# Kernel optimization log

Hardware: AMD Instinct MI355X
Metric: run time of the kernel (lower is better)

## Reference

```python
import jax, jax.numpy as jnp
import numpy as np

B, T, D_IN, H, C = 1024, 85, 20, 1024, 27
OBJ = T * 36  # flattened (T, 12, 3) object stream


def _mlp(h, W1, b1, W2, b2):
    # BaseEncoderDecoderLayout stand-in: Dense(H, relu) -> Dense(out)
    return jnp.maximum(h @ W1 + b1, 0.0) @ W2 + b2


def setup_inputs() -> dict:
    key = jax.random.key(0)
    ks = jax.random.split(key, 8)
    s = lambda k, shape: jax.random.normal(k, shape, jnp.float32) * 0.02
    return {
        "o": jax.random.normal(ks[0], (B, OBJ), jnp.float32),
        "x": jax.random.normal(ks[1], (B, T, D_IN), jnp.float32),
        # objProcess = BaseEncoderDecoderLayout(num_hid, dim_output=num_hid)
        "oW1": s(ks[2], (OBJ, H)), "ob1": jnp.zeros((H,), jnp.float32),
        "oW2": s(ks[3], (H, H)), "ob2": jnp.zeros((H,), jnp.float32),
        # expertWeightNet = BaseEncoderDecoderLayout(num_hid, dim_output=num_classes)
        "eW1": s(ks[4], (D_IN + H, H)), "eb1": jnp.zeros((H,), jnp.float32),
        "eW2": s(ks[5], (H, C)), "eb2": jnp.zeros((C,), jnp.float32),
    }


def reference(o, x, oW1, ob1, oW2, ob2, eW1, eb1, eW2, eb2):
    objInfo = _mlp(o, oW1, ob1, oW2, ob2)  # [B, H]

    def expert(cur):  # cur: [B, D_IN]
        return _mlp(jnp.concatenate([cur, objInfo], axis=-1), eW1, eb1, eW2, eb2)

    # step 0 uses raw x[:, 0, :]
    ew0 = expert(x[:, 0, :])  # [B, C]

    # steps 1..T-2: first feature of currentInput is replaced by previous
    # result's channel-0, i.e. result[:, -1, 0] -> sequential recurrence
    def step(prev, xt):  # prev: [B], xt: [B, D_IN]
        cur = jnp.concatenate([prev[:, None], xt[:, 1:]], axis=-1)
        ew = expert(cur)
        return ew[:, 0], ew

    xs = jnp.swapaxes(x[:, 1:T - 1, :], 0, 1)  # [T-2, B, D_IN]
    _, rest = jax.lax.scan(step, ew0[:, 0], xs)  # rest: [T-2, B, C]

    result = jnp.concatenate([ew0[None], rest], axis=0)  # [T-1, B, C]
    return jnp.swapaxes(result, 0, 1)  # [B, T-1, C]
```

## Files before the change

kernel.cpp:

```cpp
#include <hip/hip_runtime.h>
#include <hip/hip_bf16.h>

#define B_   1024
#define T_   85
#define DIN  20
#define H_   1024
#define C_   27
#define OBJ_ (T_ * 36)
#define TOUT (T_ - 1)

typedef unsigned short u16;
typedef __attribute__((ext_vector_type(8))) short bf16x8;
typedef __attribute__((ext_vector_type(4))) float f32x4;

__device__ __forceinline__ u16 f2bf(float f) {
    __hip_bfloat16 h = __float2bfloat16(f);
    return *reinterpret_cast<u16*>(&h);
}
__device__ __forceinline__ float bf2f(u16 u) {
    __hip_bfloat16 h;
    *reinterpret_cast<u16*>(&h) = u;
    return __bfloat162float(h);
}
__device__ __forceinline__ int f_as_i(float f) {
    union { float f; int i; } u; u.f = f; return u.i;
}
__device__ __forceinline__ float i_as_f(int i) {
    union { float f; int i; } u; u.i = i; return u.f;
}

__device__ __forceinline__ float wave64_sum_bcast(float p) {
    p += i_as_f(__builtin_amdgcn_update_dpp(0, f_as_i(p), 0x111, 0xf, 0xf, true));
    p += i_as_f(__builtin_amdgcn_update_dpp(0, f_as_i(p), 0x112, 0xf, 0xf, true));
    p += i_as_f(__builtin_amdgcn_update_dpp(0, f_as_i(p), 0x114, 0xf, 0xf, true));
    p += i_as_f(__builtin_amdgcn_update_dpp(0, f_as_i(p), 0x118, 0xf, 0xf, true));
    p += i_as_f(__builtin_amdgcn_update_dpp(0, f_as_i(p), 0x142, 0xa, 0xf, true));
    p += i_as_f(__builtin_amdgcn_update_dpp(0, f_as_i(p), 0x143, 0xc, 0xf, true));
    return i_as_f(__builtin_amdgcn_readlane(f_as_i(p), 63));
}

__global__ __launch_bounds__(256) void convertK2(
    const float* __restrict__ o, const float* __restrict__ oW1,
    const float* __restrict__ eW1, const float* __restrict__ oW2,
    const float* __restrict__ eW2, const float* __restrict__ ob2,
    u16* __restrict__ o_bf, u16* __restrict__ bW1t, u16* __restrict__ bE1t,
    u16* __restrict__ o2bf, u16* __restrict__ w2th,
    u16* __restrict__ e1t20, float* __restrict__ biasp)
{
    __shared__ float tl[64][65];
    const int bid = blockIdx.x, t = threadIdx.x;

    if (bid < 512) {
        for (int it = 0; it < 6; ++it) {
            const int idx = (bid * 256 + t) + it * 131072;
            const int row = idx / 768, g = idx - row * 768;
            float4 v = make_float4(0.f, 0.f, 0.f, 0.f);
            if (g < 765) v = *(const float4*)(o + (size_t)row * 3060 + g * 4);
            const float* vp = (const float*)&v;
            ushort4 uh;
            uh.x = f2bf(vp[0]); uh.y = f2bf(vp[1]);
            uh.z = f2bf(vp[2]); uh.w = f2bf(vp[3]);
            *(ushort4*)(o_bf + (size_t)row * 3072 + g * 4) = uh;
        }
    } else if (bid < 1536) {
        const bool isW1 = (bid < 1280);
        const int idx = isW1 ? (bid - 512) : (bid - 1280);
        const int k0 = (idx >> 4) * 64, n0 = (idx & 15) * 64;
        const float* src = isW1 ? oW1 : (eW1 + (size_t)DIN * H_);
        const int Ksrc = isW1 ? 3060 : 1024;
        u16* dst = isW1 ? bW1t : bE1t;
        const int ldk = isW1 ? 3072 : 1024;
#pragma unroll
        for (int r = 0; r < 4; ++r) {
            const int k = k0 + r * 16 + (t >> 4);
            float4 v = make_float4(0.f, 0.f, 0.f, 0.f);
            if (k < Ksrc)
                v = *(const float4*)(src + (size_t)k * 1024 + n0 + (t & 15) * 4);
            const float* vp = (const float*)&v;
#pragma unroll
            for (int j = 0; j < 4; ++j)
                tl[r * 16 + (t >> 4)][(t & 15) * 4 + j] = vp[j];
        }
        __syncthreads();
#pragma unroll
        for (int r = 0; r < 4; ++r) {
            const int n = r * 16 + (t >> 4);
            ushort4 u;
            u.x = f2bf(tl[(t & 15) * 4 + 0][n]);
            u.y = f2bf(tl[(t & 15) * 4 + 1][n]);
            u.z = f2bf(tl[(t & 15) * 4 + 2][n]);
            u.w = f2bf(tl[(t & 15) * 4 + 3][n]);
            *(ushort4*)(dst + (size_t)(n0 + n) * ldk + k0 + (t & 15) * 4) = u;
        }
    } else if (bid < 1664) {
        const int base = (bid - 1536) * 256 + t;
#pragma unroll
        for (int it = 0; it < 8; ++it) {
            const int g = base + it * 32768;
            float4 v = *(const float4*)(oW2 + (size_t)g * 4);
            const float* vp = (const float*)&v;
            ushort4 uh;
            uh.x = f2bf(vp[0]); uh.y = f2bf(vp[1]);
            uh.z = f2bf(vp[2]); uh.w = f2bf(vp[3]);
            *(ushort4*)(o2bf + (size_t)g * 4) = uh;
        }
    } else if (bid < 1696) {
        const int c = bid - 1664;
#pragma unroll
        for (int kk = 0; kk < 4; ++kk) {
            const int k = kk * 256 + t;
            const float v = (c < C_) ? eW2[(size_t)k * C_ + c] : 0.f;
            w2th[(size_t)c * 1024 + k] = f2bf(v);
        }
    } else if (bid < 1700) {
        const int n = (bid - 1696) * 256 + t;
        u16 buf[32];
#pragma unroll
        for (int k = 0; k < 32; ++k)
            buf[k] = (k < DIN) ? f2bf(eW1[(size_t)k * H_ + n]) : (u16)0;
#pragma unroll
        for (int q = 0; q < 4; ++q)
            *(uint4*)(e1t20 + (size_t)n * 32 + q * 8) = *(uint4*)&buf[q * 8];
    } else {
        const int r = bid - 1700, kc = r >> 2, nb = r & 3;
        const int n = nb * 256 + t;
        const int k0 = kc * 128;
        float acc = 0.f;
#pragma unroll 8
        for (int k = 0; k < 128; ++k)
            acc = fmaf(ob2[k0 + k], eW1[(size_t)(DIN + k0 + k) * H_ + n], acc);
        biasp[kc * H_ + n] = acc;
    }
}

template <int BN>
__device__ __forceinline__ void gemm_mfma_tile(
    const u16* __restrict__ A0, const u16* __restrict__ Bt,
    float* __restrict__ C, const float* __restrict__ bias,
    int ldK, int nk1, int gm0, int gn0, char* lds)
{
    constexpr int FN    = BN / 32;
    constexpr int WNw   = BN / 2;
    constexpr int BR    = BN / 64;
    constexpr int BUFSZ = 8192 + BN * 64;

    const int tid  = threadIdx.x;
    const int wave = tid >> 6, l = tid & 63, ml = l & 15, koct = l >> 4;
    const int wm = wave >> 1, wn = wave & 1;
    const int swz = koct ^ ((ml >> 1) & 3);
    const int a_ro = (wm * 64 + ml) * 64 + swz * 16;
    const int b_ro = (wn * WNw + ml) * 64 + swz * 16;

    const int sm = tid >> 2, sq = tid & 3;
    int wAo[2], wBo[BR];
    size_t gAo[2], gBo[BR];
#pragma unroll
    for (int q = 0; q < 2; ++q) {
        const int m = q * 64 + sm;
        wAo[q] = m * 64 + ((sq ^ ((m >> 1) & 3)) * 16);
        gAo[q] = (size_t)(gm0 + m) * ldK * 2 + sq * 16;
    }
#pragma unroll
    for (int q = 0; q < BR; ++q) {
        const int n = q * 64 + sm;
        wBo[q] = n * 64 + ((sq ^ ((n >> 1) & 3)) * 16);
        gBo[q] = (size_t)(gn0 + n) * ldK * 2 + sq * 16;
    }

    f32x4 acc[4][FN];
    const f32x4 zz = {0.f, 0.f, 0.f, 0.f};
#pragma unroll
    for (int i = 0; i < 4; ++i)
#pragma unroll
        for (int j = 0; j < FN; ++j) acc[i][j] = zz;

    const char* A0c = (const char*)A0;
    const char* Btc = (const char*)Bt;

    uint4 st[2 + BR];
    auto stage = [&](int kt) {
        const size_t koff = (size_t)kt * 64;
        st[0] = *(const uint4*)(A0c + gAo[0] + koff);
        st[1] = *(const uint4*)(A0c + gAo[1] + koff);
#pragma unroll
        for (int q = 0; q < BR; ++q)
            st[2 + q] = *(const uint4*)(Btc + gBo[q] + koff);
    };
    auto dswrite = [&](int buf) {
        char* d = lds + buf * BUFSZ;
        *(uint4*)(d + wAo[0]) = st[0];
        *(uint4*)(d + wAo[1]) = st[1];
#pragma unroll
        for (int q = 0; q < BR; ++q)
            *(uint4*)(d + 8192 + wBo[q]) = st[2 + q];
    };
    auto compute = [&](int buf) {
        const char* As = lds + buf * BUFSZ;
        const char* Bs = As + 8192;
        bf16x8 af[4], bfv[FN];
#pragma unroll
        for (int fm = 0; fm < 4; ++fm)
            af[fm] = *(const bf16x8*)(As + a_ro + fm * 1024);
#pragma unroll
        for (int fn = 0; fn < FN; ++fn)
            bfv[fn] = *(const bf16x8*)(Bs + b_ro + fn * 1024);
#pragma unroll
        for (int fm = 0; fm < 4; ++fm)
#pragma unroll
            for (int fn = 0; fn < FN; ++fn)
                acc[fm][fn] = __builtin_amdgcn_mfma_f32_16x16x32_bf16(
                    af[fm], bfv[fn], acc[fm][fn], 0, 0, 0);
    };

    stage(0); dswrite(0); __syncthreads();
    for (int kt = 0; kt < nk1; ++kt) {
        if (kt + 1 < nk1) stage(kt + 1);
        compute(kt & 1);
        if (kt + 1 < nk1) dswrite((kt + 1) & 1);
        __syncthreads();
    }

    float br[FN];
#pragma unroll
    for (int fn = 0; fn < FN; ++fn)
        br[fn] = bias ? bias[gn0 + wn * WNw + fn * 16 + ml] : 0.f;
#pragma unroll
    for (int fm = 0; fm < 4; ++fm) {
        const int rowb = gm0 + wm * 64 + fm * 16 + koct * 4;
#pragma unroll
        for (int fn = 0; fn < FN; ++fn) {
            const int col = gn0 + wn * WNw + fn * 16 + ml;
#pragma unroll
            for (int r = 0; r < 4; ++r)
                C[(size_t)(rowb + r) * 1024 + col] = acc[fm][fn][r] + br[fn];
        }
    }
}

__global__ __launch_bounds__(256) void kernelA2(
    const u16* __restrict__ o_bf, const u16* __restrict__ bW1t,
    const u16* __restrict__ o2bf, const u16* __restrict__ bE1t,
    float* __restrict__ p_h1, float* __restrict__ p_wc)
{
    __shared__ alignas(16) char lds[2 * 12288];
    const int bid = blockIdx.x;
    if (bid < 384) {
        const int c = bid >> 7, tl = bid & 127;
        gemm_mfma_tile<64>(o_bf + c * 1024, bW1t + c * 1024,
                           p_h1 + (size_t)c * 1048576, nullptr, 3072, 32,
                           (tl >> 4) * 128, (tl & 15) * 64, lds);
    } else {
        const int tl = bid - 384;
        gemm_mfma_tile<64>(o2bf, bE1t, p_wc, nullptr, 1024, 32,
                           (tl >> 4) * 128, (tl & 15) * 64, lds);
    }
}

__global__ __launch_bounds__(256) void epilogue2(
    const float* __restrict__ p_h1, const float* __restrict__ p_wc,
    const float* __restrict__ ob1, const float* __restrict__ eb1,
    const float* __restrict__ biasp,
    u16* __restrict__ h1bf, u16* __restrict__ Wct, float* __restrict__ biasWc)
{
    __shared__ float tl[64][65];
    const int bid = blockIdx.x, t = threadIdx.x;
    if (bid < 256) {
#pragma unroll
        for (int it = 0; it < 4; ++it) {
            const int g = bid * 1024 + it * 256 + t;
            const size_t e = (size_t)g * 4;
            float4 a = *(const float4*)(p_h1 + e);
            float4 b = *(const float4*)(p_h1 + 1048576 + e);
            float4 c = *(const float4*)(p_h1 + 2097152 + e);
            float4 s = *(const float4*)(ob1 + (e & 1023));
            const float *ap = (const float*)&a, *bp = (const float*)&b,
                        *cp = (const float*)&c, *sp = (const float*)&s;
            ushort4 uh;
            u16* up = (u16*)&uh;
#pragma unroll
            for (int j = 0; j < 4; ++j)
                up[j] = f2bf(fmaxf(ap[j] + bp[j] + cp[j] + sp[j], 0.f));
            *(ushort4*)(h1bf + e) = uh;
        }
    } else if (bid < 512) {
        const int idx = bid - 256;
        const int k0 = (idx >> 4) * 64, n0 = (idx & 15) * 64;
#pragma unroll
        for (int r = 0; r < 4; ++r) {
            const int k = k0 + r * 16 + (t >> 4);
            float4 v = *(const float4*)(p_wc + (size_t)k * 1024 + n0 + (t & 15) * 4);
            const float* vp = (const float*)&v;
#pragma unroll
            for (int j = 0; j < 4; ++j)
                tl[r * 16 + (t >> 4)][(t & 15) * 4 + j] = vp[j];
        }
        __syncthreads();
#pragma unroll
        for (int r = 0; r < 4; ++r) {
            const int n = r * 16 + (t >> 4);
            ushort4 u;
            u.x = f2bf(tl[(t & 15) * 4 + 0][n]);
            u.y = f2bf(tl[(t & 15) * 4 + 1][n]);
            u.z = f2bf(tl[(t & 15) * 4 + 2][n]);
            u.w = f2bf(tl[(t & 15) * 4 + 3][n]);
            *(ushort4*)(Wct + (size_t)(n0 + n) * 1024 + k0 + (t & 15) * 4) = u;
        }
    } else {
        const int j0 = t * 4;
        float4 s = *(const float4*)(eb1 + j0);
        float* sp = (float*)&s;
#pragma unroll
        for (int kc = 0; kc < 8; ++kc) {
            float4 p = *(const float4*)(biasp + kc * H_ + j0);
            const float* pp = (const float*)&p;
#pragma unroll
            for (int i = 0; i < 4; ++i) sp[i] += pp[i];
        }
        *(float4*)(biasWc + j0) = s;
    }
}

__global__ __launch_bounds__(256) void kernelB2(
    const u16* __restrict__ h1bf, const u16* __restrict__ Wct,
    const float* __restrict__ biasWc,
    float* __restrict__ base0, float* __restrict__ base1)
{
    __shared__ alignas(16) char lds[2 * 12288];
    const int bid = blockIdx.x;
    const int p = bid >> 7, tl = bid & 127;
    gemm_mfma_tile<64>(h1bf + p * 512, Wct + p * 512,
                       p ? base1 : base0, p ? biasWc : nullptr,
                       1024, 16, (tl >> 4) * 128, (tl & 15) * 64, lds);
}

#define CPH 8
#define CNPH 11

__global__ __launch_bounds__(256, 3) void chain_seq5(
    const float* __restrict__ x, const u16* __restrict__ e1t20,
    const float* __restrict__ eW1, const float* __restrict__ eW2,
    const float* __restrict__ eb2,
    const float* __restrict__ base0, const float* __restrict__ base1,
    float* __restrict__ cur0_buf)
{
    __shared__ u16   A_bf[2][CPH * 1032];
    __shared__ float base_s[1024];

    const int b = blockIdx.x, tid = threadIdx.x;
    const int w = tid >> 6, l = tid & 63;
    const int ml = l & 15, koct = l >> 4;

    {
        const int j = tid * 4;
        float4 b0v = *(const float4*)&base0[(size_t)b * H_ + j];
        float4 b1v = *(const float4*)&base1[(size_t)b * H_ + j];
        float4 s;
        s.x = b0v.x + b1v.x; s.y = b0v.y + b1v.y;
        s.z = b0v.z + b1v.z; s.w = b0v.w + b1v.w;
        *(float4*)&base_s[j] = s;
    }
    __syncthreads();

    const f32x4 zz = {0.f, 0.f, 0.f, 0.f};

    auto produce = [&](int ph) {
        const int t0 = ph * CPH;
        u16 hw[8];
        const int tg = t0 + ml;
        const bool rowok = (ml < CPH) && (tg < T_);
#pragma unroll
        for (int e = 0; e < 8; ++e) {
            const int k = koct * 8 + e;
            float vx = 0.f;
            if (rowok && k >= 1 && k < DIN)
                vx = x[(size_t)b * (T_ * DIN) + tg * DIN + k];
            hw[e] = f2bf(vx);
        }
        bf16x8 af;
        {
            uint4 pk;
            pk.x = hw[0] | ((unsigned)hw[1] << 16);
            pk.y = hw[2] | ((unsigned)hw[3] << 16);
            pk.z = hw[4] | ((unsigned)hw[5] << 16);
            pk.w = hw[6] | ((unsigned)hw[7] << 16);
            af = *(bf16x8*)&pk;
        }
        const int beg = (w == 1) ? 0 : (w == 2) ? 22 : 43;
        const int end = (w == 1) ? 22 : (w == 2) ? 43 : 64;
        u16* dst = A_bf[ph & 1];
#pragma unroll 2
        for (int jt = beg; jt < end; ++jt) {
            const bf16x8 bf = *(const bf16x8*)
                &e1t20[(size_t)(jt * 16 + ml) * 32 + koct * 8];
            f32x4 c = __builtin_amdgcn_mfma_f32_16x16x32_bf16(af, bf, zz, 0, 0, 0);
            if (koct < 2) {
                const int jcol = jt * 16 + ml;
                const float bj = base_s[jcol];
#pragma unroll
                for (int r = 0; r < 4; ++r)
                    dst[(koct * 4 + r) * 1032 + jcol] = f2bf(c[r] + bj);
            }
        }
    };

    float u[16], v[16];
    float prev = 0.f, cur0_init = 0.f;
    if (w) {
        produce(0);
    } else {
#pragma unroll
        for (int i = 0; i < 16; ++i) {
            const int j = i * 64 + l;
            u[i] = eW1[j];
            v[i] = eW2[(size_t)j * C_];
        }
        cur0_init = x[(size_t)b * (T_ * DIN)];
    }
    __syncthreads();

    const float eb20 = eb2[0];
    float* cb = cur0_buf + (size_t)b * TOUT;

#pragma unroll 1
    for (int ph = 0; ph < CNPH; ++ph) {
        if (w) {
            if (ph + 1 < CNPH) produce(ph + 1);
        } else {
            const int t0 = ph * CPH;
            const int rem = 83 - t0;
            const int nst = (rem < CPH) ? rem : CPH;
            const u16* Abuf = A_bf[ph & 1];

            float a_cur[16];
#pragma unroll
            for (int i = 0; i < 16; ++i)
                a_cur[i] = bf2f(Abuf[i * 64 + l]);

            for (int sl = 0; sl < nst; ++sl) {
                const int t = t0 + sl;
                const int sln = (sl + 1 < nst) ? sl + 1 : sl;
                float a_nxt[16];
#pragma unroll
                for (int i = 0; i < 16; ++i)
                    a_nxt[i] = bf2f(Abuf[sln * 1032 + i * 64 + l]);

                const float cur0 = (t == 0) ? cur0_init : prev;
                if (l == 0) cb[t] = cur0;

                float p0 = 0.f, p1 = 0.f, p2 = 0.f, p3 = 0.f;
#pragma unroll
                for (int i = 0; i < 16; i += 4) {
                    p0 = fmaf(fmaxf(fmaf(cur0, u[i + 0], a_cur[i + 0]), 0.f), v[i + 0], p0);
                    p1 = fmaf(fmaxf(fmaf(cur0, u[i + 1], a_cur[i + 1]), 0.f), v[i + 1], p1);
                    p2 = fmaf(fmaxf(fmaf(cur0, u[i + 2], a_cur[i + 2]), 0.f), v[i + 2], p2);
                    p3 = fmaf(fmaxf(fmaf(cur0, u[i + 3], a_cur[i + 3]), 0.f), v[i + 3], p3);
                }
                const float p = (p0 + p1) + (p2 + p3);
                prev = eb20 + wave64_sum_bcast(p);

#pragma unroll
                for (int i = 0; i < 16; ++i) a_cur[i] = a_nxt[i];
            }
        }
        __syncthreads();
    }
    if (w == 0 && l == 0) cb[TOUT - 1] = prev;
}

__global__ __launch_bounds__(256, 4) void expand(
    const float* __restrict__ x, const float* __restrict__ base0,
    const float* __restrict__ base1, const float* __restrict__ cur0_buf,
    const u16* __restrict__ e1t20, const u16* __restrict__ w2th,
    const float* __restrict__ eb2, float* __restrict__ out)
{
    __shared__ u16 A_lds[64 * 32];
    __shared__ u16 e_lds[128 * 32];
    __shared__ u16 h_lds[64 * 128];
    __shared__ u16 w2_s[32 * 128];
    __shared__ float base_s[2 * 128];

    const int tid = threadIdx.x;
    const int g0 = blockIdx.x * 64;
    const int w = tid >> 6, l = tid & 63, ml = l & 15, koct = l >> 4;
    const int b0 = g0 / 84;
    const int b1 = (b0 + 1 < B_) ? b0 + 1 : b0;

    {
        const int row = tid >> 2, q = tid & 3;
        const int g = g0 + row, bb = g / 84, tt = g - bb * 84;
        u16 hw[8];
#pragma unroll
        for (int c = 0; c < 8; ++c) {
            const int k = q * 8 + c;
            float v = 0.f;
            if (k == 0) v = cur0_buf[g];
            else if (k < DIN) v = x[(size_t)bb * (T_ * DIN) + tt * DIN + k];
            hw[c] = f2bf(v);
        }
        uint4 pk;
        pk.x = hw[0] | ((unsigned)hw[1] << 16);
        pk.y = hw[2] | ((unsigned)hw[3] << 16);
        pk.z = hw[4] | ((unsigned)hw[5] << 16);
        pk.w = hw[6] | ((unsigned)hw[7] << 16);
        *(uint4*)&A_lds[row * 32 + q * 8] = pk;
    }

    const int grow = w * 16 + ml;
    const int g = g0 + grow;
    const int sel = g / 84 - b0;
    __syncthreads();
    const bf16x8 xfrag = *(const bf16x8*)&A_lds[grow * 32 + koct * 8];

    f32x4 acc[2];
    const f32x4 zz = {0.f, 0.f, 0.f, 0.f};
    acc[0] = zz; acc[1] = zz;

#pragma unroll 1
    for (int kc = 0; kc < 8; ++kc) {
        const int n0 = kc * 128;
        if (kc) __syncthreads();
        {
            const u16* src = e1t20 + n0 * 32 + tid * 16;
            *(uint4*)&e_lds[tid * 16]     = *(const uint4*)src;
            *(uint4*)&e_lds[tid * 16 + 8] = *(const uint4*)(src + 8);
        }
        {
            const int wr = tid >> 3, sg = tid & 7;
            const u16* srcw = w2th + (size_t)wr * 1024 + n0 + sg * 16;
            const int s0 = (sg * 2) ^ (wr & 15), s1 = (sg * 2 + 1) ^ (wr & 15);
            *(uint4*)&w2_s[wr * 128 + s0 * 8] = *(const uint4*)srcw;
            *(uint4*)&w2_s[wr * 128 + s1 * 8] = *(const uint4*)(srcw + 8);
        }
        {
            const int bs = tid >> 7, c = tid & 127;
            const size_t rb = (size_t)(bs ? b1 : b0) * H_ + n0 + c;
            base_s[bs * 128 + c] = base0[rb] + base1[rb];
        }
        __syncthreads();

#pragma unroll
        for (int p = 0; p < 8; ++p) {
            const bf16x8 ef = *(const bf16x8*)&e_lds[(p * 16 + ml) * 32 + koct * 8];
            f32x4 c1 = zz;
            c1 = __builtin_amdgcn_mfma_f32_16x16x32_bf16(ef, xfrag, c1, 0, 0, 0);
            u16 hq[4];
#pragma unroll
            for (int q = 0; q < 4; ++q) {
                const int j = p * 16 + koct * 4 + q;
                const float v = c1[q] + base_s[sel * 128 + j];
                hq[q] = f2bf(fmaxf(v, 0.f));
            }
            uint2 pk;
            pk.x = hq[0] | ((unsigned)hq[1] << 16);
            pk.y = hq[2] | ((unsigned)hq[3] << 16);
            const int s16 = (p * 2 + (koct >> 1)) ^ ml;
            *(uint2*)&h_lds[grow * 128 + s16 * 8 + (koct & 1) * 4] = pk;
        }

#pragma unroll
        for (int ks = 0; ks < 4; ++ks) {
            const int sl = (((ks * 4 + koct) ^ ml)) * 8;
            const bf16x8 hf = *(const bf16x8*)&h_lds[grow * 128 + sl];
#pragma unroll
            for (int ct = 0; ct < 2; ++ct) {
                const bf16x8 wf = *(const bf16x8*)&w2_s[(ct * 16 + ml) * 128 + sl];
                acc[ct] = __builtin_amdgcn_mfma_f32_16x16x32_bf16(
                    wf, hf, acc[ct], 0, 0, 0);
            }
        }
    }

#pragma unroll
    for (int ct = 0; ct < 2; ++ct) {
#pragma unroll
        for (int q = 0; q < 4; ++q) {
            const int c = ct * 16 + koct * 4 + q;
            if (c < C_)
                out[(size_t)g * C_ + c] = acc[ct][q] + eb2[c];
        }
    }
}

struct GemmSmem {
    float As[2][16][68];
    float Bs[2][16][64];
};

template <int RELU>
__device__ __forceinline__ void gemm_core(
    const float* __restrict__ A, int lda,
    const float* __restrict__ Bm, int ldb,
    const float* __restrict__ bias, const float* __restrict__ bias_parts,
    float* __restrict__ Cc, int ldc, int K, int tile, GemmSmem& sm)
{
    const int tid = threadIdx.x;
    const int bm = (tile >> 4) * 64, bn = (tile & 15) * 64;
    const int wave = tid >> 6, l = tid & 63;
    const int n0 = (wave & 1) * 32 + (l & 7) * 4;
    const int m0 = (wave >> 1) * 32 + (l >> 3) * 4;
    const int am = tid >> 2, akq = tid & 3;
    const int bk = tid >> 4, bnq = tid & 15;
    const float* Arow = A + (size_t)(bm + am) * lda + akq * 4;
    const float* Brow = Bm + (size_t)bk * ldb + bn + bnq * 4;
    float acc[4][4] = {};
    const int nIter = (K + 15) >> 4;
    {
        const int ak = akq * 4;
        float4 av = (ak + 4 <= K) ? *(const float4*)(Arow)
                                  : make_float4(0.f, 0.f, 0.f, 0.f);
        float4 bv = (bk < K) ? *(const float4*)(Brow)
                             : make_float4(0.f, 0.f, 0.f, 0.f);
        sm.As[0][akq * 4 + 0][am] = av.x; sm.As[0][akq * 4 + 1][am] = av.y;
        sm.As[0][akq * 4 + 2][am] = av.z; sm.As[0][akq * 4 + 3][am] = av.w;
        *(float4*)&sm.Bs[0][bk][bnq * 4] = bv;
    }
    __syncthreads();
    for (int it = 0; it < nIter; ++it) {
        const int cur = it & 1;
        const bool pf = (it + 1 < nIter);
        float4 pav, pbv;
        if (pf) {
            const int k0 = (it + 1) << 4, ak = k0 + akq * 4;
            pav = (ak + 4 <= K) ? *(const float4*)(Arow + k0)
                                : make_float4(0.f, 0.f, 0.f, 0.f);
            pbv = (k0 + bk < K) ? *(const float4*)(Brow + (size_t)k0 * ldb)
                                : make_float4(0.f, 0.f, 0.f, 0.f);
        }
#pragma unroll
        for (int kk = 0; kk < 16; ++kk) {
            float ar[4], br[4];
            *(float4*)ar = *(const float4*)&sm.As[cur][kk][m0];
            *(float4*)br = *(const float4*)&sm.Bs[cur][kk][n0];
#pragma unroll
            for (int r = 0; r < 4; ++r)
#pragma unroll
                for (int c = 0; c < 4; ++c)
                    acc[r][c] = fmaf(ar[r], br[c], acc[r][c]);
        }
        if (pf) {
            const int nb = cur ^ 1;
            sm.As[nb][akq * 4 + 0][am] = pav.x; sm.As[nb][akq * 4 + 1][am] = pav.y;
            sm.As[nb][akq * 4 + 2][am] = pav.z; sm.As[nb][akq * 4 + 3][am] = pav.w;
            *(float4*)&sm.Bs[nb][bk][bnq * 4] = pbv;
        }
        __syncthreads();
    }
    float bias4[4];
#pragma unroll
    for (int c = 0; c < 4; ++c) {
        const int col = bn + n0 + c;
        float b = bias ? bias[col] : 0.f;
        if (bias_parts)
#pragma unroll
            for (int p = 0; p < 8; ++p) b += bias_parts[p * H_ + col];
        bias4[c] = b;
    }
#pragma unroll
    for (int r = 0; r < 4; ++r) {
        float4 v; float* vp = (float*)&v;
#pragma unroll
        for (int c = 0; c < 4; ++c) {
            float t2 = acc[r][c] + bias4[c];
            if (RELU) t2 = fmaxf(t2, 0.f);
            vp[c] = t2;
        }
        *(float4*)&Cc[(size_t)(bm + m0 + r) * ldc + bn + n0] = v;
    }
}

__global__ __launch_bounds__(256) void kernelA_fb(
    const float* __restrict__ o, const float* __restrict__ oW1,
    const float* __restrict__ ob1, const float* __restrict__ oW2,
    const float* __restrict__ eW1, const float* __restrict__ ob2,
    float* __restrict__ h1, float* __restrict__ Wc, float* __restrict__ biasc)
{
    __shared__ GemmSmem sm;
    const int bid = blockIdx.x;
    if (bid < 256) {
        gemm_core<1>(o, OBJ_, oW1, H_, ob1, nullptr, h1, H_, OBJ_, bid, sm);
    } else if (bid < 512) {
        gemm_core<0>(oW2, H_, eW1 + (size_t)DIN * H_, H_, nullptr, nullptr,
                     Wc, H_, H_, bid - 256, sm);
    } else {
        const int r = bid - 512, kc = r >> 2, nb = r & 3;
        const int n = nb * 256 + (int)threadIdx.x;
        const int k0 = kc * 128;
        float acc = 0.f;
#pragma unroll 8
        for (int k = 0; k < 128; ++k)
            acc = fmaf(ob2[k0 + k], eW1[(size_t)(DIN + k0 + k) * H_ + n], acc);
        biasc[kc * H_ + n] = acc;
    }
}

__global__ __launch_bounds__(256) void kernelB_fb(
    const float* __restrict__ h1, const float* __restrict__ Wc,
    const float* __restrict__ eb1, const float* __restrict__ biasc,
    float* __restrict__ base0)
{
    __shared__ GemmSmem sm;
    gemm_core<0>(h1, H_, Wc, H_, eb1, biasc, base0, H_, H_, blockIdx.x, sm);
}

__global__ __launch_bounds__(256, 2) void expert_seq_fb(
    const float* __restrict__ x, const float* __restrict__ eW1,
    const float* __restrict__ eW2, const float* __restrict__ eb2,
    const float* __restrict__ base0, float* __restrict__ out)
{
    const int b   = blockIdx.x;
    const int tid = threadIdx.x;
    const int j0  = tid * 4;

    __shared__ float xl[T_ * DIN];
    __shared__ float pl[256 * 29];
    __shared__ float pl2[256];
    __shared__ float prevs;

    for (int idx = tid; idx < T_ * DIN; idx += 256)
        xl[idx] = x[(size_t)b * (T_ * DIN) + idx];

    float w1r[DIN][4];
#pragma unroll
    for (int d = 0; d < DIN; ++d)
        *(float4*)w1r[d] = *(const float4*)&eW1[(size_t)d * H_ + j0];

    float base_r[4];
    *(float4*)base_r = *(const float4*)&base0[(size_t)b * H_ + j0];

    float w2r[4][C_];
#pragma unroll
    for (int i = 0; i < 4; ++i)
#pragma unroll
        for (int c = 0; c < C_; ++c)
            w2r[i][c] = eW2[(size_t)(j0 + i) * C_ + c];

    const float myb = (tid < C_) ? eb2[tid] : 0.f;
    __syncthreads();

    float prev = 0.f;
#pragma unroll 1
    for (int t = 0; t < TOUT; ++t) {
        const float cur0 = (t == 0) ? xl[0] : prev;
        float h[4];
#pragma unroll
        for (int i = 0; i < 4; ++i)
            h[i] = fmaf(cur0, w1r[0][i], base_r[i]);
#pragma unroll
        for (int d = 1; d < DIN; ++d) {
            const float xv = xl[t * DIN + d];
#pragma unroll
            for (int i = 0; i < 4; ++i)
                h[i] = fmaf(xv, w1r[d][i], h[i]);
        }
#pragma unroll
        for (int i = 0; i < 4; ++i)
            h[i] = fmaxf(h[i], 0.f);
        float p[C_];
#pragma unroll
        for (int c = 0; c < C_; ++c)
            p[c] = h[0] * w2r[0][c];
#pragma unroll
        for (int i = 1; i < 4; ++i)
#pragma unroll
            for (int c = 0; c < C_; ++c)
                p[c] = fmaf(h[i], w2r[i][c], p[c]);
#pragma unroll
        for (int c = 0; c < C_; ++c)
            pl[tid * 29 + c] = p[c];
        __syncthreads();
        {
            const int c2 = tid & 31, grp = tid >> 5;
            float s = 0.f;
            if (c2 < C_) {
                const int basei = grp * 32 * 29 + c2;
#pragma unroll
                for (int s2 = 0; s2 < 32; ++s2)
                    s += pl[basei + s2 * 29];
            }
            pl2[tid] = s;
        }
        __syncthreads();
        if (tid < C_) {
            float o = myb;
#pragma unroll
            for (int g = 0; g < 8; ++g)
                o += pl2[g * 32 + tid];
            out[((size_t)b * TOUT + t) * C_ + tid] = o;
            if (tid == 0) prevs = o;
        }
        __syncthreads();
        prev = prevs;
    }
}

extern "C" void kernel_launch(void* const* d_in, const int* in_sizes, int n_in,
                              void* d_out, int out_size, void* d_ws, size_t ws_size,
                              hipStream_t stream)
{
    const float* o   = (const float*)d_in[0];
    const float* x   = (const float*)d_in[1];
    const float* oW1 = (const float*)d_in[2];
    const float* ob1 = (const float*)d_in[3];
    const float* oW2 = (const float*)d_in[4];
    const float* ob2 = (const float*)d_in[5];
    const float* eW1 = (const float*)d_in[6];
    const float* eb1 = (const float*)d_in[7];
    const float* eW2 = (const float*)d_in[8];
    const float* eb2 = (const float*)d_in[9];

    float* outp = (float*)d_out;
    float* ws   = (float*)d_ws;
    dim3 blk(256);

    const size_t NEED2 = 38326272;
    if (ws_size >= NEED2) {
        float* p_h1   = ws;
        float* p_wc   = ws + 3145728;
        float* biasWc = ws + 4194304;
        float* cur0b  = ws + 4195328;
        float* biasp  = ws + 4281344;
        u16*   ub     = (u16*)(ws + 4289536);
        u16 *o_bf  = ub,             *bW1t = ub + 3145728;
        u16 *bE1t  = ub + 6291456,   *o2bf = ub + 7340032;
        u16 *h1bf  = ub + 8388608,   *Wct  = ub + 9437184;
        u16 *w2th  = ub + 10485760;
        u16 *e1t20 = ub + 10551296;
        float* base0 = p_h1;
        float* base1 = p_h1 + 1048576;

        convertK2<<<dim3(1732), blk, 0, stream>>>(o, oW1, eW1, oW2, eW2, ob2,
                                                  o_bf, bW1t, bE1t, o2bf,
                                                  w2th, e1t20, biasp);
        kernelA2<<<dim3(512), blk, 0, stream>>>(o_bf, bW1t, o2bf, bE1t,
                                                p_h1, p_wc);
        epilogue2<<<dim3(513), blk, 0, stream>>>(p_h1, p_wc, ob1, eb1, biasp,
                                                 h1bf, Wct, biasWc);
        kernelB2<<<dim3(256), blk, 0, stream>>>(h1bf, Wct, biasWc,
                                                base0, base1);
        chain_seq5<<<dim3(B_), blk, 0, stream>>>(x, e1t20, eW1, eW2, eb2,
                                                 base0, base1, cur0b);
        expand<<<dim3(1344), blk, 0, stream>>>(x, base0, base1, cur0b, e1t20,
                                               w2th, eb2, outp);
    } else {
        const size_t MF = (size_t)H_ * H_;
        float* h1    = ws;
        float* Wc    = ws + MF;
        float* base0 = ws + 2 * MF;
        float* biasc = outp;
        kernelA_fb<<<dim3(544), blk, 0, stream>>>(o, oW1, ob1, oW2, eW1, ob2,
                                                  h1, Wc, biasc);
        kernelB_fb<<<dim3(256), blk, 0, stream>>>(h1, Wc, eb1, biasc, base0);
        expert_seq_fb<<<dim3(B_), blk, 0, stream>>>(x, eW1, eW2, eb2,
                                                    base0, outp);
    }
}
```

Before: 165.7 us.

## Restructure recurrence kernel: serialize produce/consume phases, register-cache weights, vectorized LDS

Replaces the double-buffered producer/consumer chain kernel with a single-buffer scheme. The producer waves now compute 16 timesteps per phase into LDS and then synchronize, instead of overlapping with the consumer. The B-operand e1t20 slices are held in registers, x is staged once into LDS, and the bias add moves into registers on the consumer side. The consumer now reads its A rows through 16-byte vectorized LDS loads in a contiguous per-lane layout. This removes the global x reloads and scattered 2-byte LDS reads and allows occupancy 4, but it gives up producer/consumer overlap and uses many registers for ereg.

```diff
diff --git a/kernel.cpp b/kernel.cpp
--- a/kernel.cpp
+++ b/kernel.cpp
@@ -333,86 +333,59 @@
                        1024, 16, (tl >> 4) * 128, (tl & 15) * 64, lds);
 }
 
-#define CPH 8
-#define CNPH 11
-
-__global__ __launch_bounds__(256, 3) void chain_seq5(
+#define CPH6  16
+#define CNPH6 6
+#define ASTR  1048
+#define APL   528
+
+__global__ __launch_bounds__(256, 4) void chain_seq6(
     const float* __restrict__ x, const u16* __restrict__ e1t20,
     const float* __restrict__ eW1, const float* __restrict__ eW2,
     const float* __restrict__ eb2,
     const float* __restrict__ base0, const float* __restrict__ base1,
     float* __restrict__ cur0_buf)
 {
-    __shared__ u16   A_bf[2][CPH * 1032];
-    __shared__ float base_s[1024];
+    __shared__ alignas(16) u16 A_bf[CPH6 * ASTR];
+    __shared__ float xl[T_ * DIN];
 
     const int b = blockIdx.x, tid = threadIdx.x;
     const int w = tid >> 6, l = tid & 63;
     const int ml = l & 15, koct = l >> 4;
 
-    {
-        const int j = tid * 4;
-        float4 b0v = *(const float4*)&base0[(size_t)b * H_ + j];
-        float4 b1v = *(const float4*)&base1[(size_t)b * H_ + j];
-        float4 s;
-        s.x = b0v.x + b1v.x; s.y = b0v.y + b1v.y;
-        s.z = b0v.z + b1v.z; s.w = b0v.w + b1v.w;
-        *(float4*)&base_s[j] = s;
-    }
-    __syncthreads();
+    for (int i = tid; i < T_ * DIN; i += 256)
+        xl[i] = x[(size_t)b * (T_ * DIN) + i];
 
     const f32x4 zz = {0.f, 0.f, 0.f, 0.f};
 
-    auto produce = [&](int ph) {
-        const int t0 = ph * CPH;
-        u16 hw[8];
-        const int tg = t0 + ml;
-        const bool rowok = (ml < CPH) && (tg < T_);
-#pragma unroll
-        for (int e = 0; e < 8; ++e) {
-            const int k = koct * 8 + e;
-            float vx = 0.f;
-            if (rowok && k >= 1 && k < DIN)
-                vx = x[(size_t)b * (T_ * DIN) + tg * DIN + k];
-            hw[e] = f2bf(vx);
-        }
-        bf16x8 af;
-        {
-            uint4 pk;
-            pk.x = hw[0] | ((unsigned)hw[1] << 16);
-            pk.y = hw[2] | ((unsigned)hw[3] << 16);
-            pk.z = hw[4] | ((unsigned)hw[5] << 16);
-            pk.w = hw[6] | ((unsigned)hw[7] << 16);
-            af = *(bf16x8*)&pk;
-        }
-        const int beg = (w == 1) ? 0 : (w == 2) ? 22 : 43;
-        const int end = (w == 1) ? 22 : (w == 2) ? 43 : 64;
-        u16* dst = A_bf[ph & 1];
-#pragma unroll 2
-        for (int jt = beg; jt < end; ++jt) {
-            const bf16x8 bf = *(const bf16x8*)
-                &e1t20[(size_t)(jt * 16 + ml) * 32 + koct * 8];
-            f32x4 c = __builtin_amdgcn_mfma_f32_16x16x32_bf16(af, bf, zz, 0, 0, 0);
-            if (koct < 2) {
-                const int jcol = jt * 16 + ml;
-                const float bj = base_s[jcol];
-#pragma unroll
-                for (int r = 0; r < 4; ++r)
-                    dst[(koct * 4 + r) * 1032 + jcol] = f2bf(c[r] + bj);
-            }
-        }
-    };
-
-    float u[16], v[16];
+    bf16x8 ereg[22];
+    if (w) {
+#pragma unroll
+        for (int q = 0; q < 22; ++q) {
+            const int jt = (w - 1) + 3 * q;
+            if (jt < 64)
+                ereg[q] = *(const bf16x8*)
+                    &e1t20[(size_t)(jt * 16 + ml) * 32 + koct * 8];
+        }
+    }
+
+    float u[16], v[16], baseR[16];
     float prev = 0.f, cur0_init = 0.f;
-    if (w) {
-        produce(0);
-    } else {
-#pragma unroll
-        for (int i = 0; i < 16; ++i) {
-            const int j = i * 64 + l;
-            u[i] = eW1[j];
-            v[i] = eW2[(size_t)j * C_];
+    if (w == 0) {
+        const int j0 = l * 16;
+#pragma unroll
+        for (int i = 0; i < 16; i += 4)
+            *(float4*)&u[i] = *(const float4*)&eW1[j0 + i];
+#pragma unroll
+        for (int i = 0; i < 16; ++i)
+            v[i] = eW2[(size_t)(j0 + i) * C_];
+#pragma unroll
+        for (int i = 0; i < 16; i += 4) {
+            float4 b0v = *(const float4*)&base0[(size_t)b * H_ + j0 + i];
+            float4 b1v = *(const float4*)&base1[(size_t)b * H_ + j0 + i];
+            baseR[i + 0] = b0v.x + b1v.x;
+            baseR[i + 1] = b0v.y + b1v.y;
+            baseR[i + 2] = b0v.z + b1v.z;
+            baseR[i + 3] = b0v.w + b1v.w;
         }
         cur0_init = x[(size_t)b * (T_ * DIN)];
     }
@@ -420,29 +393,69 @@
 
     const float eb20 = eb2[0];
     float* cb = cur0_buf + (size_t)b * TOUT;
+    int t = 0;
 
 #pragma unroll 1
-    for (int ph = 0; ph < CNPH; ++ph) {
+    for (int ph = 0; ph < CNPH6; ++ph) {
+        const int t0 = ph * CPH6;
+
         if (w) {
-            if (ph + 1 < CNPH) produce(ph + 1);
-        } else {
-            const int t0 = ph * CPH;
+            u16 hw[8];
+            const int tg = t0 + ml;
+#pragma unroll
+            for (int e = 0; e < 8; ++e) {
+                const int k = koct * 8 + e;
+                float vx = 0.f;
+                if (k >= 1 && k < DIN && tg < T_) vx = xl[tg * DIN + k];
+                hw[e] = f2bf(vx);
+            }
+            bf16x8 af;
+            {
+                uint4 pk;
+                pk.x = hw[0] | ((unsigned)hw[1] << 16);
+                pk.y = hw[2] | ((unsigned)hw[3] << 16);
+                pk.z = hw[4] | ((unsigned)hw[5] << 16);
+                pk.w = hw[6] | ((unsigned)hw[7] << 16);
+                af = *(bf16x8*)&pk;
+            }
+            const int wbase = (ml >> 3) * APL + (ml & 7);
+#pragma unroll
+            for (int q = 0; q < 22; ++q) {
+                const int jt = (w - 1) + 3 * q;
+                if (jt < 64) {
+                    f32x4 c = __builtin_amdgcn_mfma_f32_16x16x32_bf16(
+                        af, ereg[q], zz, 0, 0, 0);
+#pragma unroll
+                    for (int r = 0; r < 4; ++r) {
+                        const int row = koct * 4 + r;
+                        A_bf[row * ASTR + wbase + jt * 8] = f2bf(c[r]);
+                    }
+                }
+            }
+        }
+        __syncthreads();
+
+        if (w == 0) {
             const int rem = 83 - t0;
-            const int nst = (rem < CPH) ? rem : CPH;
-            const u16* Abuf = A_bf[ph & 1];
-
-            float a_cur[16];
-#pragma unroll
-            for (int i = 0; i < 16; ++i)
-                a_cur[i] = bf2f(Abuf[i * 64 + l]);
-
-            for (int sl = 0; sl < nst; ++sl) {
-                const int t = t0 + sl;
+            const int nst = (rem < CPH6) ? rem : CPH6;
+
+            uint4 ra = *(const uint4*)&A_bf[l * 8];
+            uint4 rb = *(const uint4*)&A_bf[APL + l * 8];
+            float ab[16];
+            {
+                const u16* pa = (const u16*)&ra;
+                const u16* pb = (const u16*)&rb;
+#pragma unroll
+                for (int i = 0; i < 8; ++i) {
+                    ab[i]     = bf2f(pa[i]) + baseR[i];
+                    ab[8 + i] = bf2f(pb[i]) + baseR[8 + i];
+                }
+            }
+
+            for (int sl = 0; sl < nst; ++sl, ++t) {
                 const int sln = (sl + 1 < nst) ? sl + 1 : sl;
-                float a_nxt[16];
-#pragma unroll
-                for (int i = 0; i < 16; ++i)
-                    a_nxt[i] = bf2f(Abuf[sln * 1032 + i * 64 + l]);
+                uint4 rna = *(const uint4*)&A_bf[sln * ASTR + l * 8];
+                uint4 rnb = *(const uint4*)&A_bf[sln * ASTR + APL + l * 8];
 
                 const float cur0 = (t == 0) ? cur0_init : prev;
                 if (l == 0) cb[t] = cur0;
@@ -450,16 +463,22 @@
                 float p0 = 0.f, p1 = 0.f, p2 = 0.f, p3 = 0.f;
 #pragma unroll
                 for (int i = 0; i < 16; i += 4) {
-                    p0 = fmaf(fmaxf(fmaf(cur0, u[i + 0], a_cur[i + 0]), 0.f), v[i + 0], p0);
-                    p1 = fmaf(fmaxf(fmaf(cur0, u[i + 1], a_cur[i + 1]), 0.f), v[i + 1], p1);
-                    p2 = fmaf(fmaxf(fmaf(cur0, u[i + 2], a_cur[i + 2]), 0.f), v[i + 2], p2);
-                    p3 = fmaf(fmaxf(fmaf(cur0, u[i + 3], a_cur[i + 3]), 0.f), v[i + 3], p3);
+                    p0 = fmaf(fmaxf(fmaf(cur0, u[i + 0], ab[i + 0]), 0.f), v[i + 0], p0);
+                    p1 = fmaf(fmaxf(fmaf(cur0, u[i + 1], ab[i + 1]), 0.f), v[i + 1], p1);
+                    p2 = fmaf(fmaxf(fmaf(cur0, u[i + 2], ab[i + 2]), 0.f), v[i + 2], p2);
+                    p3 = fmaf(fmaxf(fmaf(cur0, u[i + 3], ab[i + 3]), 0.f), v[i + 3], p3);
                 }
-                const float p = (p0 + p1) + (p2 + p3);
-                prev = eb20 + wave64_sum_bcast(p);
-
-#pragma unroll
-                for (int i = 0; i < 16; ++i) a_cur[i] = a_nxt[i];
+                prev = eb20 + wave64_sum_bcast((p0 + p1) + (p2 + p3));
+
+                {
+                    const u16* pa = (const u16*)&rna;
+                    const u16* pb = (const u16*)&rnb;
+#pragma unroll
+                    for (int i = 0; i < 8; ++i) {
+                        ab[i]     = bf2f(pa[i]) + baseR[i];
+                        ab[8 + i] = bf2f(pb[i]) + baseR[8 + i];
+                    }
+                }
             }
         }
         __syncthreads();
@@ -837,7 +856,7 @@
                                                  h1bf, Wct, biasWc);
         kernelB2<<<dim3(256), blk, 0, stream>>>(h1bf, Wct, biasWc,
                                                 base0, base1);
-        chain_seq5<<<dim3(B_), blk, 0, stream>>>(x, e1t20, eW1, eW2, eb2,
+        chain_seq6<<<dim3(B_), blk, 0, stream>>>(x, e1t20, eW1, eW2, eb2,
                                                  base0, base1, cur0b);
         expand<<<dim3(1344), blk, 0, stream>>>(x, base0, base1, cur0b, e1t20,
                                                w2th, eb2, outp);
```

Result: faster. 161.3 us (-2.6%).
